# Kernel tuning notes

Measured on AMD Instinct MI355X. Metric: run time of the kernel, lower is better.

The kernel has to match this reference:

```python
import jax, jax.numpy as jnp
import numpy as np

VOCAB = 1000000
EMBED_DIM = 64


def setup_inputs() -> dict:
    key = jax.random.key(0)
    embeddings = jax.random.normal(key, (VOCAB, EMBED_DIM), dtype=jnp.float32)
    return {"embeddings": embeddings, "user_id": 12345, "top_n": 10}


def reference(embeddings, user_id, top_n):
    # target_embedding = embedding_layer(user_id): [d]
    target = embeddings[user_id]  # [d]
    # cosine_similarity(target[None, :], all_embeddings): [V]
    dot = embeddings @ target  # [V]
    norm_t = jnp.linalg.norm(target)  # scalar (norm over axis=-1 of [1, d])
    norm_all = jnp.linalg.norm(embeddings, axis=-1)  # [V]
    sims = dot / (norm_t * norm_all)
    # tf.nn.top_k with k = top_n + 1, then drop the first (self) match
    top_vals, top_idx = jax.lax.top_k(sims, top_n + 1)
    return top_vals[1:], top_idx[1:]
```

## Files before the change

kernel.cpp:

```cpp
#include <hip/hip_runtime.h>
#include <cmath>
#include <climits>

#define EMBED 64
#define KTOP 11
#define NB   512
#define BLOCK1 128
#define NW1  (BLOCK1 / 64)
#define BLOCK2 256
#define NW2  (BLOCK2 / 64)
#define TILE_BYTES 16384

typedef const __attribute__((address_space(1))) void gv_t;
typedef __attribute__((address_space(3))) void lv_t;

__device__ __forceinline__ void topk_insert(float (&vals)[KTOP], int (&idxs)[KTOP],
                                            float v, int i) {
  float last = vals[KTOP - 1];
  if (v < last) return;
  if (v == last && i >= idxs[KTOP - 1]) return;
  float cv = v; int ci = i;
#pragma unroll
  for (int j = 0; j < KTOP; ++j) {
    bool better = (cv > vals[j]) || (cv == vals[j] && ci < idxs[j]);
    if (better) {
      float tv = vals[j]; int ti = idxs[j];
      vals[j] = cv; idxs[j] = ci;
      cv = tv; ci = ti;
    }
  }
}

__device__ __forceinline__ void wave_merge(float (&vals)[KTOP], int (&idxs)[KTOP],
                                           float* wv, int* wi, int lane) {
#pragma unroll
  for (int round = 0; round < KTOP; ++round) {
    float v = vals[0]; int i = idxs[0]; int l = lane;
#pragma unroll
    for (int off = 32; off > 0; off >>= 1) {
      float ov = __shfl_xor(v, off, 64);
      int   oi = __shfl_xor(i, off, 64);
      int   ol = __shfl_xor(l, off, 64);
      if (ov > v || (ov == v && oi < i)) { v = ov; i = oi; l = ol; }
    }
    if (l == lane) {
#pragma unroll
      for (int j = 0; j < KTOP - 1; ++j) { vals[j] = vals[j + 1]; idxs[j] = idxs[j + 1]; }
      vals[KTOP - 1] = -INFINITY; idxs[KTOP - 1] = INT_MAX;
    }
    if (lane == 0) { wv[round] = v; wi[round] = i; }
  }
}

__device__ __forceinline__ void dma_tile(const char* g, size_t byteBase,
                                         int lane, char* lds) {
#pragma unroll
  for (int j = 0; j < 16; ++j) {
    __builtin_amdgcn_global_load_lds(
        (gv_t*)(g + byteBase + (size_t)j * 1024 + (size_t)lane * 16),
        (lv_t*)(lds + j * 1024), 16, 0, 0);
  }
}

__device__ __forceinline__ void dma_tile_clamped(const char* g, size_t byteBase,
                                                 int lane, char* lds, size_t maxOff) {
#pragma unroll
  for (int j = 0; j < 16; ++j) {
    size_t off = byteBase + (size_t)j * 1024 + (size_t)lane * 16;
    if (off > maxOff) off = maxOff;
    __builtin_amdgcn_global_load_lds(
        (gv_t*)(g + off), (lv_t*)(lds + j * 1024), 16, 0, 0);
  }
}

__global__ __launch_bounds__(BLOCK1) void sim_pass1(
    const float* __restrict__ emb, const int* __restrict__ user_id,
    float* __restrict__ cand_val, int* __restrict__ cand_idx, int V) {
  __shared__ __align__(16) char smem[2 * NW1 * TILE_BYTES];

  const int lane = threadIdx.x & 63;
  const int wid  = threadIdx.x >> 6;
  const int uid  = *user_id;

  const float4* trow = (const float4*)(emb + (size_t)uid * EMBED);
  float4 tv[16];
#pragma unroll
  for (int j = 0; j < 16; ++j) tv[j] = trow[(j + lane) & 15];

  float vals[KTOP]; int idxs[KTOP];
#pragma unroll
  for (int j = 0; j < KTOP; ++j) { vals[j] = -INFINITY; idxs[j] = INT_MAX; }

  const int gw = blockIdx.x * NW1 + wid;
  const int nW = NB * NW1;
  const int nTiles = (V + 63) >> 6;
  const char* g = (const char*)emb;
  const size_t maxOff = (size_t)V * 256 - 16;
  char* myLds = smem + wid * (2 * TILE_BYTES);

  int p = 0;
  int tile = gw;
  if (tile < nTiles) {
    if (((size_t)tile * 64 + 64) * 256 - 16 <= maxOff + 0)
      dma_tile(g, (size_t)tile << 14, lane, myLds);
    else
      dma_tile_clamped(g, (size_t)tile << 14, lane, myLds, maxOff);
  }

  for (; tile < nTiles; tile += nW) {
    const int next = tile + nW;
    const bool pf = next < nTiles;
    if (pf) {
      char* nb = myLds + ((p ^ 1) * TILE_BYTES);
      if ((size_t)(next + 1) * 64 * 256 - 16 <= maxOff)
        dma_tile(g, (size_t)next << 14, lane, nb);
      else
        dma_tile_clamped(g, (size_t)next << 14, lane, nb, maxOff);
      asm volatile("s_waitcnt vmcnt(16)" ::: "memory");
    } else {
      asm volatile("s_waitcnt vmcnt(0)" ::: "memory");
    }

    const char* lb = myLds + p * TILE_BYTES + lane * 256;
    float dot = 0.f, nr = 0.f;
#pragma unroll
    for (int j = 0; j < 16; ++j) {
      const int c = (j + lane) & 15;
      float4 v = *(const float4*)(lb + c * 16);
      float4 t = tv[j];
      dot = fmaf(v.x, t.x, dot); dot = fmaf(v.y, t.y, dot);
      dot = fmaf(v.z, t.z, dot); dot = fmaf(v.w, t.w, dot);
      nr  = fmaf(v.x, v.x, nr);  nr  = fmaf(v.y, v.y, nr);
      nr  = fmaf(v.z, v.z, nr);  nr  = fmaf(v.w, v.w, nr);
    }
    const int row = (tile << 6) + lane;
    if (row < V)
      topk_insert(vals, idxs, dot / sqrtf(nr), row);
    p ^= 1;
  }

  __syncthreads();
  float* wv = (float*)smem;
  int*   wi = (int*)(smem + NW1 * KTOP * sizeof(float));
  wave_merge(vals, idxs, &wv[wid * KTOP], &wi[wid * KTOP], lane);
  __syncthreads();

  if (wid == 0) {
    float v = (lane < NW1 * KTOP) ? wv[lane] : -INFINITY;
    int   i = (lane < NW1 * KTOP) ? wi[lane] : INT_MAX;
#pragma unroll
    for (int round = 0; round < KTOP; ++round) {
      float bv = v; int bi = i; int bl = lane;
#pragma unroll
      for (int off = 32; off > 0; off >>= 1) {
        float ov = __shfl_xor(bv, off, 64);
        int   oi = __shfl_xor(bi, off, 64);
        int   ol = __shfl_xor(bl, off, 64);
        if (ov > bv || (ov == bv && oi < bi)) { bv = ov; bi = oi; bl = ol; }
      }
      if (bl == lane) { v = -INFINITY; i = INT_MAX; }
      if (lane == 0) {
        cand_val[blockIdx.x * KTOP + round] = bv;
        cand_idx[blockIdx.x * KTOP + round] = bi;
      }
    }
  }
}

__global__ __launch_bounds__(BLOCK2) void sim_pass2(
    const float* __restrict__ emb, const int* __restrict__ user_id,
    const float* __restrict__ cand_val, const int* __restrict__ cand_idx,
    float* __restrict__ out, int topn, int ncand) {
  __shared__ float wv[NW2 * KTOP];
  __shared__ int   wi[NW2 * KTOP];
  __shared__ float s_nt;

  const int lane = threadIdx.x & 63;
  const int wid  = threadIdx.x >> 6;

  if (wid == 0) {
    const int uid = *user_id;
    float x = (lane < EMBED) ? emb[(size_t)uid * EMBED + lane] : 0.f;
    float s = x * x;
#pragma unroll
    for (int off = 32; off > 0; off >>= 1) s += __shfl_xor(s, off, 64);
    if (lane == 0) s_nt = sqrtf(s);
  }

  float vals[KTOP]; int idxs[KTOP];
#pragma unroll
  for (int j = 0; j < KTOP; ++j) { vals[j] = -INFINITY; idxs[j] = INT_MAX; }

  for (int c = threadIdx.x; c < ncand; c += BLOCK2)
    topk_insert(vals, idxs, cand_val[c], cand_idx[c]);

  wave_merge(vals, idxs, &wv[wid * KTOP], &wi[wid * KTOP], lane);
  __syncthreads();

  if (wid == 0) {
    float v = (lane < NW2 * KTOP) ? wv[lane] : -INFINITY;
    int   i = (lane < NW2 * KTOP) ? wi[lane] : INT_MAX;
    const float nt = s_nt;
#pragma unroll
    for (int round = 0; round < KTOP; ++round) {
      float bv = v; int bi = i; int bl = lane;
#pragma unroll
      for (int off = 32; off > 0; off >>= 1) {
        float ov = __shfl_xor(bv, off, 64);
        int   oi = __shfl_xor(bi, off, 64);
        int   ol = __shfl_xor(bl, off, 64);
        if (ov > bv || (ov == bv && oi < bi)) { bv = ov; bi = oi; bl = ol; }
      }
      if (bl == lane) { v = -INFINITY; i = INT_MAX; }
      if (lane == 0 && round >= 1 && round <= topn) {
        out[round - 1]        = bv / nt;
        out[topn + round - 1] = (float)bi;
      }
    }
  }
}

extern "C" void kernel_launch(void* const* d_in, const int* in_sizes, int n_in,
                              void* d_out, int out_size, void* d_ws, size_t ws_size,
                              hipStream_t stream) {
  const float* emb = (const float*)d_in[0];
  const int*   uid = (const int*)d_in[1];
  const int V    = in_sizes[0] / EMBED;
  const int topn = out_size / 2;

  float* cand_val = (float*)d_ws;
  int*   cand_idx = (int*)((char*)d_ws + (size_t)NB * KTOP * sizeof(float));

  sim_pass1<<<NB, BLOCK1, 0, stream>>>(emb, uid, cand_val, cand_idx, V);
  sim_pass2<<<1, BLOCK2, 0, stream>>>(emb, uid, cand_val, cand_idx,
                                      (float*)d_out, topn, NB * KTOP);
}
```

Baseline: 407.3 us.

## Split each row across two half-waves with smaller tiles and larger blocks

Each wave now handles 32-row tiles, and each half-wave computes half of a row's dot product and norm. The halves are combined with a cross-lane shuffle, and the two halves take turns doing the top-k insert each iteration. Block size doubles to 256 threads with a per-CU occupancy hint, and the DMA wait count is adjusted to the smaller tile. The aim is more waves and loads in flight and a lower per-lane register footprint. The cost is more loop iterations, extra shuffles, and half the lanes sitting idle during the insert.

```diff
diff --git a/kernel.cpp b/kernel.cpp
--- a/kernel.cpp
+++ b/kernel.cpp
@@ -5,11 +5,13 @@
 #define EMBED 64
 #define KTOP 11
 #define NB   512
-#define BLOCK1 128
+#define BLOCK1 256
 #define NW1  (BLOCK1 / 64)
 #define BLOCK2 256
 #define NW2  (BLOCK2 / 64)
-#define TILE_BYTES 16384
+#define TROWS 32
+#define TILE_BYTES (TROWS * 256)
+#define TILE_DMA   (TILE_BYTES / 1024)
 
 typedef const __attribute__((address_space(1))) void gv_t;
 typedef __attribute__((address_space(3))) void lv_t;
@@ -55,7 +57,7 @@
 __device__ __forceinline__ void dma_tile(const char* g, size_t byteBase,
                                          int lane, char* lds) {
 #pragma unroll
-  for (int j = 0; j < 16; ++j) {
+  for (int j = 0; j < TILE_DMA; ++j) {
     __builtin_amdgcn_global_load_lds(
         (gv_t*)(g + byteBase + (size_t)j * 1024 + (size_t)lane * 16),
         (lv_t*)(lds + j * 1024), 16, 0, 0);
@@ -65,7 +67,7 @@
 __device__ __forceinline__ void dma_tile_clamped(const char* g, size_t byteBase,
                                                  int lane, char* lds, size_t maxOff) {
 #pragma unroll
-  for (int j = 0; j < 16; ++j) {
+  for (int j = 0; j < TILE_DMA; ++j) {
     size_t off = byteBase + (size_t)j * 1024 + (size_t)lane * 16;
     if (off > maxOff) off = maxOff;
     __builtin_amdgcn_global_load_lds(
@@ -73,7 +75,7 @@
   }
 }
 
-__global__ __launch_bounds__(BLOCK1) void sim_pass1(
+__global__ __launch_bounds__(BLOCK1, 2) void sim_pass1(
     const float* __restrict__ emb, const int* __restrict__ user_id,
     float* __restrict__ cand_val, int* __restrict__ cand_idx, int V) {
   __shared__ __align__(16) char smem[2 * NW1 * TILE_BYTES];
@@ -81,11 +83,13 @@
   const int lane = threadIdx.x & 63;
   const int wid  = threadIdx.x >> 6;
   const int uid  = *user_id;
+  const int row  = lane & 31;
+  const int half = lane >> 5;
 
   const float4* trow = (const float4*)(emb + (size_t)uid * EMBED);
-  float4 tv[16];
-#pragma unroll
-  for (int j = 0; j < 16; ++j) tv[j] = trow[(j + lane) & 15];
+  float4 tv[8];
+#pragma unroll
+  for (int j = 0; j < 8; ++j) tv[j] = trow[half * 8 + ((j + lane) & 7)];
 
   float vals[KTOP]; int idxs[KTOP];
 #pragma unroll
@@ -93,7 +97,7 @@
 
   const int gw = blockIdx.x * NW1 + wid;
   const int nW = NB * NW1;
-  const int nTiles = (V + 63) >> 6;
+  const int nTiles = (V + TROWS - 1) / TROWS;
   const char* g = (const char*)emb;
   const size_t maxOff = (size_t)V * 256 - 16;
   char* myLds = smem + wid * (2 * TILE_BYTES);
@@ -101,41 +105,43 @@
   int p = 0;
   int tile = gw;
   if (tile < nTiles) {
-    if (((size_t)tile * 64 + 64) * 256 - 16 <= maxOff + 0)
-      dma_tile(g, (size_t)tile << 14, lane, myLds);
+    if ((size_t)(tile + 1) * TILE_BYTES - 16 <= maxOff)
+      dma_tile(g, (size_t)tile * TILE_BYTES, lane, myLds);
     else
-      dma_tile_clamped(g, (size_t)tile << 14, lane, myLds, maxOff);
-  }
-
-  for (; tile < nTiles; tile += nW) {
+      dma_tile_clamped(g, (size_t)tile * TILE_BYTES, lane, myLds, maxOff);
+  }
+
+  int par = 0;
+  for (; tile < nTiles; tile += nW, par ^= 1) {
     const int next = tile + nW;
-    const bool pf = next < nTiles;
-    if (pf) {
+    if (next < nTiles) {
       char* nb = myLds + ((p ^ 1) * TILE_BYTES);
-      if ((size_t)(next + 1) * 64 * 256 - 16 <= maxOff)
-        dma_tile(g, (size_t)next << 14, lane, nb);
+      if ((size_t)(next + 1) * TILE_BYTES - 16 <= maxOff)
+        dma_tile(g, (size_t)next * TILE_BYTES, lane, nb);
       else
-        dma_tile_clamped(g, (size_t)next << 14, lane, nb, maxOff);
-      asm volatile("s_waitcnt vmcnt(16)" ::: "memory");
+        dma_tile_clamped(g, (size_t)next * TILE_BYTES, lane, nb, maxOff);
+      asm volatile("s_waitcnt vmcnt(8)" ::: "memory");
     } else {
       asm volatile("s_waitcnt vmcnt(0)" ::: "memory");
     }
 
-    const char* lb = myLds + p * TILE_BYTES + lane * 256;
+    const char* lb = myLds + p * TILE_BYTES + row * 256 + half * 128;
     float dot = 0.f, nr = 0.f;
 #pragma unroll
-    for (int j = 0; j < 16; ++j) {
-      const int c = (j + lane) & 15;
-      float4 v = *(const float4*)(lb + c * 16);
+    for (int j = 0; j < 8; ++j) {
+      float4 v = *(const float4*)(lb + ((j + lane) & 7) * 16);
       float4 t = tv[j];
       dot = fmaf(v.x, t.x, dot); dot = fmaf(v.y, t.y, dot);
       dot = fmaf(v.z, t.z, dot); dot = fmaf(v.w, t.w, dot);
       nr  = fmaf(v.x, v.x, nr);  nr  = fmaf(v.y, v.y, nr);
       nr  = fmaf(v.z, v.z, nr);  nr  = fmaf(v.w, v.w, nr);
     }
-    const int row = (tile << 6) + lane;
-    if (row < V)
-      topk_insert(vals, idxs, dot / sqrtf(nr), row);
+    dot += __shfl_xor(dot, 32, 64);
+    nr  += __shfl_xor(nr,  32, 64);
+
+    const int r = tile * TROWS + row;
+    if (half == par && r < V)
+      topk_insert(vals, idxs, dot / sqrtf(nr), r);
     p ^= 1;
   }
 
```

After: 402.7 us. Within noise of the previous version (-1.1%).
